# Kernel optimization log

Hardware: AMD Instinct MI355X
Metric: run time of the kernel (lower is better)

The kernel has to match this reference:

```python
import jax, jax.numpy as jnp
import numpy as np

B, T, E, H = 2, 2048, 1024, 16
D = E // H            # head dim = 64
ROT = D // 2          # rotary_dim = 32 (only first half of head dim is rotated)
THETA = 10000.0


def _rope(x):
    # x: (B, H, T, D). Faithful to rotary_embedding_torch.rotate_queries_or_keys
    # with dim=ROT: rotate first ROT features, interleaved-pair style, pass rest.
    t = x.shape[-2]
    inv = 1.0 / (THETA ** (jnp.arange(0, ROT, 2, dtype=jnp.float32) / ROT))   # (ROT//2,)
    freqs = jnp.arange(t, dtype=jnp.float32)[:, None] * inv[None, :]          # (T, ROT//2)
    freqs = jnp.repeat(freqs, 2, axis=-1)                                      # (T, ROT)
    cos, sin = jnp.cos(freqs), jnp.sin(freqs)
    xr, xp = x[..., :ROT], x[..., ROT:]
    p = xr.reshape(*xr.shape[:-1], ROT // 2, 2)
    rot = jnp.stack((-p[..., 1], p[..., 0]), axis=-1).reshape(xr.shape)
    return jnp.concatenate([xr * cos + rot * sin, xp], axis=-1)


def setup_inputs() -> dict:
    key = jax.random.key(0)
    k1, k2, k3 = jax.random.split(key, 3)
    query = jax.random.normal(k1, (B, T, E), dtype=jnp.float32)
    inputs = {
        "query": query,
        "key": query,            # ignored (cross_attention=False)
        "value": query,          # ignored
        "padding_mask": jnp.ones((B, T), dtype=bool),
        "in_proj_weight": jax.random.uniform(k2, (3 * E, E), dtype=jnp.float32),
        "out_proj_weight": jax.random.normal(k3, (E, E), dtype=jnp.float32) * (E ** -0.5),
    }
    return inputs


def reference(query, key, value, padding_mask, in_proj_weight, out_proj_weight):
    # cross_attention=False: key/value are overwritten by query
    key = query
    value = query
    q = query @ in_proj_weight[:E].T
    k = key @ in_proj_weight[E:2 * E].T
    v = value @ in_proj_weight[2 * E:].T
    # NOTE: raw reshape (B,T,E)->(B,H,T,D), exactly as in the torch module
    q = q.reshape(B, H, T, D)
    k = k.reshape(B, H, T, D)
    v = v.reshape(B, H, T, D)
    q = _rope(q)
    k = _rope(k)   # causal self-attention path: rotate keys too
    causal = jnp.tril(jnp.ones((T, T), dtype=bool))                 # (T, T)
    mask = causal[None, None] & padding_mask[:, None, None, :]      # (B,1,T,T) -> broadcast over H
    scores = jnp.einsum("bhqd,bhkd->bhqk", q, k) / jnp.sqrt(jnp.float32(D))
    scores = jnp.where(mask, scores, -jnp.inf)
    attn = jax.nn.softmax(scores, axis=-1)
    x = jnp.einsum("bhqk,bhkd->bhqd", attn, v)
    x = x.reshape(B, T, E)      # raw reshape back, as in torch
    return x @ out_proj_weight.T
```

## Files before the change

### kernel.cpp

```cpp
#include <hip/hip_runtime.h>
#include <stdint.h>

#define T_ 2048
#define E_ 1024

typedef __attribute__((ext_vector_type(8))) __bf16 bf16x8;
typedef __attribute__((ext_vector_type(4))) float f32x4;

__device__ __forceinline__ void gload_lds16(const void* g, void* l) {
  __builtin_amdgcn_global_load_lds(
      (const __attribute__((address_space(1))) unsigned int*)g,
      (__attribute__((address_space(3))) unsigned int*)l, 16, 0, 0);
}

__global__ __launch_bounds__(256) void k_prep(const float4* __restrict__ q,
                                              ushort4* __restrict__ xh,
                                              ushort4* __restrict__ xl,
                                              const float4* __restrict__ win,
                                              ushort4* __restrict__ whh,
                                              ushort4* __restrict__ whl,
                                              const float4* __restrict__ wout,
                                              ushort4* __restrict__ wob,
                                              float2* __restrict__ cs) {
  const int b = blockIdx.x, tid = threadIdx.x;
  if (b < 7168) {
    const float4* src;
    ushort4 *hi, *lo;
    int i;
    if (b < 4096) { src = q; hi = xh; lo = xl; i = b * 256 + tid; }
    else          { src = win; hi = whh; lo = whl; i = (b - 4096) * 256 + tid; }
    float4 x = src[i];
    float xs[4] = {x.x, x.y, x.z, x.w};
    union { __bf16 bb[4]; ushort4 u; } H, L;
#pragma unroll
    for (int jj = 0; jj < 4; ++jj) {
      __bf16 h = (__bf16)xs[jj];
      H.bb[jj] = h;
      L.bb[jj] = (__bf16)(xs[jj] - (float)h);
    }
    hi[i] = H.u;
    lo[i] = L.u;
  } else if (b < 8192) {
    int i = (b - 7168) * 256 + tid;
    float4 x = wout[i];
    float xs[4] = {x.x, x.y, x.z, x.w};
    union { __bf16 bb[4]; ushort4 u; } H;
#pragma unroll
    for (int jj = 0; jj < 4; ++jj) H.bb[jj] = (__bf16)xs[jj];
    wob[i] = H.u;
  } else {
    int i = (b - 8192) * 256 + tid;
    int t = i >> 4, f = i & 15;
    double inv = pow(10000.0, -(double)f / 16.0);
    double ang = (double)t * inv;
    cs[i] = make_float2((float)cos(ang), (float)sin(ang));
  }
}

__global__ __launch_bounds__(256) void k_gemmqk(const __bf16* __restrict__ Ah,
                                                const __bf16* __restrict__ Al,
                                                const __bf16* __restrict__ Bh,
                                                const __bf16* __restrict__ Bl,
                                                int K,
                                                const float2* __restrict__ cs,
                                                __bf16* __restrict__ qhi,
                                                __bf16* __restrict__ qlo,
                                                __bf16* __restrict__ khi,
                                                __bf16* __restrict__ klo) {
  __shared__ __align__(16) __bf16 AsH[128 * 64];
  __shared__ __align__(16) __bf16 BsH[128 * 64];
  __shared__ __align__(16) __bf16 AsL[128 * 64];
  __shared__ __align__(16) __bf16 BsL[128 * 64];
  const int bi = blockIdx.x;
  const int bx = (bi >> 3) & 15;
  const int by = ((bi & 7) << 2) | ((bi >> 7) & 3);
  const int tid = threadIdx.x, lane = tid & 63, w = tid >> 6;
  const int wm = w >> 1, wn = w & 1;
  const int g = lane >> 4, d = lane & 15;
  const int m0 = by * 128, n0 = bx * 128;

  f32x4 acc[4][4];
#pragma unroll
  for (int i = 0; i < 4; ++i)
#pragma unroll
    for (int j = 0; j < 4; ++j) acc[i][j] = (f32x4)(0.0f);

  const int lr8 = lane >> 3;
  const int swz8 = ((lane & 7) ^ lr8) * 8;
  const int rsl = (d & 7);

  for (int k0 = 0; k0 < K; k0 += 64) {
    __syncthreads();
#pragma unroll
    for (int c = 0; c < 4; ++c) {
      const int rr = c * 32 + w * 8 + lr8;
      const int ldo = (c * 32 + w * 8) * 64;
      gload_lds16(Ah + (size_t)(m0 + rr) * K + k0 + swz8, &AsH[ldo]);
      gload_lds16(Al + (size_t)(m0 + rr) * K + k0 + swz8, &AsL[ldo]);
      gload_lds16(Bh + (size_t)(n0 + rr) * K + k0 + swz8, &BsH[ldo]);
      gload_lds16(Bl + (size_t)(n0 + rr) * K + k0 + swz8, &BsL[ldo]);
    }
    __syncthreads();
#pragma unroll
    for (int k2 = 0; k2 < 2; ++k2) {
      const int sl = ((k2 * 4 + g) ^ rsl) * 8;
      bf16x8 bh[4], bl[4];
#pragma unroll
      for (int j = 0; j < 4; ++j) {
        const int r = wn * 64 + j * 16 + d;
        bh[j] = *(const bf16x8*)&BsH[r * 64 + sl];
        bl[j] = *(const bf16x8*)&BsL[r * 64 + sl];
      }
#pragma unroll
      for (int i = 0; i < 4; ++i) {
        const int r = wm * 64 + i * 16 + d;
        const bf16x8 ahf = *(const bf16x8*)&AsH[r * 64 + sl];
        const bf16x8 alf = *(const bf16x8*)&AsL[r * 64 + sl];
#pragma unroll
        for (int j = 0; j < 4; ++j) {
          acc[i][j] = __builtin_amdgcn_mfma_f32_16x16x32_bf16(ahf, bh[j], acc[i][j], 0, 0, 0);
          acc[i][j] = __builtin_amdgcn_mfma_f32_16x16x32_bf16(alf, bh[j], acc[i][j], 0, 0, 0);
          acc[i][j] = __builtin_amdgcn_mfma_f32_16x16x32_bf16(ahf, bl[j], acc[i][j], 0, 0, 0);
        }
      }
    }
  }

#pragma unroll
  for (int i = 0; i < 4; ++i) {
    const int rbase = m0 + wm * 64 + i * 16 + g * 4;
#pragma unroll
    for (int j = 0; j < 4; ++j) {
      const int col = n0 + wn * 64 + j * 16 + d;
#pragma unroll
      for (int r = 0; r < 4; ++r) {
        const float vv = acc[i][j][r];
        const int row = rbase + r;
        const float xp = __shfl_xor(vv, 1);
        const int which = col >> 10;
        const int cl = col & 1023;
        const int d2 = cl & 63;
        const int t2 = (row & 127) * 16 + (cl >> 6);
        float y;
        if (d2 < 32) {
          const float2 cse = cs[t2 * 16 + (d2 >> 1)];
          y = (d2 & 1) ? (vv * cse.x + xp * cse.y) : (vv * cse.x - xp * cse.y);
        } else {
          y = vv;
        }
        if (which == 0) y *= 0.18033688011112042f;
        const __bf16 hi = (__bf16)y;
        const __bf16 lo = (__bf16)(y - (float)hi);
        const size_t off = (size_t)row * 1024 + cl;
        (which ? khi : qhi)[off] = hi;
        (which ? klo : qlo)[off] = lo;
      }
    }
  }
}

template <int EPI>
__global__ __launch_bounds__(256) void k_gemm64(const __bf16* __restrict__ Ah,
                                                const __bf16* __restrict__ Bh,
                                                int N, int K,
                                                __bf16* __restrict__ vt,
                                                float* __restrict__ C32) {
  __shared__ __align__(16) __bf16 As[64 * 64];
  __shared__ __align__(16) __bf16 Bs[128 * 64];
  const int bi = blockIdx.x;
  const int bx = (bi >> 3) & 7;
  const int by = ((bi & 7) << 3) | ((bi >> 6) & 7);
  const int tid = threadIdx.x, lane = tid & 63, w = tid >> 6;
  const int g = lane >> 4, d = lane & 15;
  const int m0 = by * 64, n0 = bx * 128;

  f32x4 acc[4][2];
#pragma unroll
  for (int i = 0; i < 4; ++i)
#pragma unroll
    for (int j = 0; j < 2; ++j) acc[i][j] = (f32x4)(0.0f);

  const int lr8 = lane >> 3;
  const int swz8 = ((lane & 7) ^ lr8) * 8;
  const int rsl = (d & 7);

  for (int k0 = 0; k0 < K; k0 += 64) {
    __syncthreads();
#pragma unroll
    for (int c = 0; c < 2; ++c) {
      const int rr = c * 32 + w * 8 + lr8;
      gload_lds16(Ah + (size_t)(m0 + rr) * K + k0 + swz8, &As[(c * 32 + w * 8) * 64]);
    }
#pragma unroll
    for (int c = 0; c < 4; ++c) {
      const int rr = c * 32 + w * 8 + lr8;
      gload_lds16(Bh + (size_t)(n0 + rr) * K + k0 + swz8, &Bs[(c * 32 + w * 8) * 64]);
    }
    __syncthreads();
#pragma unroll
    for (int k2 = 0; k2 < 2; ++k2) {
      const int sl = ((k2 * 4 + g) ^ rsl) * 8;
      bf16x8 bh[2], ah[4];
#pragma unroll
      for (int j = 0; j < 2; ++j)
        bh[j] = *(const bf16x8*)&Bs[(w * 32 + j * 16 + d) * 64 + sl];
#pragma unroll
      for (int i = 0; i < 4; ++i)
        ah[i] = *(const bf16x8*)&As[(i * 16 + d) * 64 + sl];
#pragma unroll
      for (int i = 0; i < 4; ++i)
#pragma unroll
        for (int j = 0; j < 2; ++j)
          acc[i][j] = __builtin_amdgcn_mfma_f32_16x16x32_bf16(ah[i], bh[j], acc[i][j], 0, 0, 0);
    }
  }

#pragma unroll
  for (int i = 0; i < 4; ++i) {
    const int rbase = m0 + i * 16 + g * 4;
#pragma unroll
    for (int j = 0; j < 2; ++j) {
      const int col = n0 + w * 32 + j * 16 + d;
#pragma unroll
      for (int r = 0; r < 4; ++r) {
        const int row = rbase + r;
        if constexpr (EPI == 1) {
          C32[(size_t)row * N + col] = acc[i][j][r];
        } else {
          const int p = row >> 7;
          const int tp = ((row & 127) << 4) | (col >> 6);
          const int dp = col & 63;
          vt[((size_t)p * 64 + dp) * 2048 + tp] = (__bf16)acc[i][j][r];
        }
      }
    }
  }
}

__global__ __launch_bounds__(512, 4) void k_attn(const __bf16* __restrict__ qhi,
                                                 const __bf16* __restrict__ qlo,
                                                 const __bf16* __restrict__ khi,
                                                 const __bf16* __restrict__ klo,
                                                 const __bf16* __restrict__ v16t,
                                                 __bf16* __restrict__ x16,
                                                 float* __restrict__ po,
                                                 float* __restrict__ pm,
                                                 float* __restrict__ pl_) {
  __shared__ __align__(16) __bf16 KH[2][64 * 64];
  __shared__ __align__(16) __bf16 KL[2][64 * 64];
  __shared__ __align__(16) __bf16 VT[2][64 * 64];
  __shared__ __align__(16) __bf16 PL[8][16 * 72];

  const int bi = blockIdx.x;
  const int b = (bi >> 3) & 15;
  const int panel = (bi & 7) | (((bi >> 7) & 3) << 3);
  const int u0 = 9 * b;
  int qtA = 0;
  while (2 * (qtA + 1) * (qtA + 2) <= u0) ++qtA;
  const int cumA = 2 * qtA * (qtA + 1);
  const int cumB = 2 * (qtA + 1) * (qtA + 2);
  const int jloA = u0 - cumA;
  const bool two = (u0 + 9 > cumB);
  const int jhiA = two ? (cumB - 1 - cumA) : (u0 + 8 - cumA);
  const int jhiB = u0 + 8 - cumB;

  const int tid = threadIdx.x, lane = tid & 63, w = tid >> 6;
  const int g = lane >> 4, d = lane & 15;
  const size_t hb = (size_t)panel * T_ * 64;

  const int kr = tid >> 3, kc = tid & 7;
  const int swz = (kc ^ (kr & 7)) * 8;
  const __bf16* kB = khi + hb;
  const __bf16* lB = klo + hb;
  const __bf16* vB = v16t + (size_t)panel * (64 * T_);

#define STAGE(j, bb)                                                        \
  {                                                                         \
    gload_lds16(kB + (size_t)((j) * 64 + kr) * 64 + swz, &KH[bb][w * 512]); \
    gload_lds16(lB + (size_t)((j) * 64 + kr) * 64 + swz, &KL[bb][w * 512]); \
    gload_lds16(vB + (size_t)kr * T_ + (j) * 64 + swz, &VT[bb][w * 512]);   \
  }

  int cur = 0;
  STAGE(jloA, 0);

  for (int seg = 0; seg < 2; ++seg) {
    if (seg && !two) break;
    const int qt = qtA + seg;
    const int jlo = seg ? 0 : jloA;
    const int jhi = seg ? jhiB : jhiA;
    const int q0 = qt << 8;

    bf16x8 qh[2][2], ql[2][2];
#pragma unroll
    for (int rb = 0; rb < 2; ++rb) {
      const int rbi = w * 2 + rb;
      const size_t qrow = hb + (size_t)(q0 + rbi * 16 + d) * 64;
      qh[rb][0] = *(const bf16x8*)&qhi[qrow + g * 8];
      qh[rb][1] = *(const bf16x8*)&qhi[qrow + 32 + g * 8];
      ql[rb][0] = *(const bf16x8*)&qlo[qrow + g * 8];
      ql[rb][1] = *(const bf16x8*)&qlo[qrow + 32 + g * 8];
    }

    f32x4 o[2][4];
#pragma unroll
    for (int rb = 0; rb < 2; ++rb)
#pragma unroll
      for (int i = 0; i < 4; ++i) o[rb][i] = (f32x4)(0.0f);
    float m_[2] = {-__builtin_inff(), -__builtin_inff()};
    float l_[2] = {0.0f, 0.0f};

    for (int j = jlo; j <= jhi; ++j) {
      __syncthreads();
      if (j < jhi) {
        STAGE(j + 1, cur ^ 1);
      } else if (!seg && two) {
        STAGE(0, cur ^ 1);
      }

#pragma unroll
      for (int rb = 0; rb < 2; ++rb) {
        const int rbi = w * 2 + rb;
        const int qrow0 = q0 + rbi * 16;
        if (j * 64 > qrow0 + 15) continue;

        f32x4 s[4];
        __builtin_amdgcn_s_setprio(1);
#pragma unroll
        for (int f = 0; f < 4; ++f) {
          f32x4 accs = (f32x4)(0.0f);
          const int colr = f * 16 + d;
#pragma unroll
          for (int ds = 0; ds < 2; ++ds) {
            const int slot = ((ds * 4 + g) ^ (colr & 7)) * 8;
            const bf16x8 kf = *(const bf16x8*)&KH[cur][colr * 64 + slot];
            const bf16x8 lf = *(const bf16x8*)&KL[cur][colr * 64 + slot];
            accs = __builtin_amdgcn_mfma_f32_16x16x32_bf16(kf, qh[rb][ds], accs, 0, 0, 0);
            accs = __builtin_amdgcn_mfma_f32_16x16x32_bf16(kf, ql[rb][ds], accs, 0, 0, 0);
            accs = __builtin_amdgcn_mfma_f32_16x16x32_bf16(lf, qh[rb][ds], accs, 0, 0, 0);
          }
          s[f] = accs;
        }
        __builtin_amdgcn_s_setprio(0);

        if (j * 64 + 63 > qrow0) {
          const int qq = qrow0 + d;
#pragma unroll
          for (int f = 0; f < 4; ++f)
#pragma unroll
            for (int r = 0; r < 4; ++r) {
              const int kv = j * 64 + f * 16 + g * 4 + r;
              if (kv > qq) s[f][r] = -30000.0f;
            }
        }

        float pmax = fmaxf(fmaxf(s[0][0], s[0][1]), fmaxf(s[0][2], s[0][3]));
#pragma unroll
        for (int f = 1; f < 4; ++f)
          pmax = fmaxf(pmax, fmaxf(fmaxf(s[f][0], s[f][1]), fmaxf(s[f][2], s[f][3])));
        pmax = fmaxf(pmax, __shfl_xor(pmax, 16));
        pmax = fmaxf(pmax, __shfl_xor(pmax, 32));

        if (!__all(pmax - m_[rb] <= 11.5f)) {
          const float mnew = fmaxf(m_[rb], pmax);
          const float fac = exp2f(m_[rb] - mnew);
          m_[rb] = mnew;
          float facr[4];
#pragma unroll
          for (int r = 0; r < 4; ++r)
            facr[r] = __shfl(fac, (lane & 48) | (g * 4 + r));
#pragma unroll
          for (int ni = 0; ni < 4; ++ni)
#pragma unroll
            for (int r = 0; r < 4; ++r) o[rb][ni][r] *= facr[r];
          l_[rb] *= fac;
        }

        float sum = 0.0f;
#pragma unroll
        for (int f = 0; f < 4; ++f) {
          union { __bf16 bb[4]; ushort4 u4; } pk;
#pragma unroll
          for (int r = 0; r < 4; ++r) {
            const float pv = exp2f(s[f][r] - m_[rb]);
            sum += pv;
            pk.bb[r] = (__bf16)pv;
          }
          *(ushort4*)&PL[w][d * 72 + f * 16 + g * 4] = pk.u4;
        }
        sum += __shfl_xor(sum, 16);
        sum += __shfl_xor(sum, 32);
        l_[rb] += sum;

        __builtin_amdgcn_s_setprio(1);
#pragma unroll
        for (int ks = 0; ks < 2; ++ks) {
          const bf16x8 pa = *(const bf16x8*)&PL[w][d * 72 + ks * 32 + g * 8];
#pragma unroll
          for (int ni = 0; ni < 4; ++ni) {
            const bf16x8 vf =
                *(const bf16x8*)&VT[cur][(ni * 16 + d) * 64 + (((ks * 4 + g) ^ (d & 7)) * 8)];
            o[rb][ni] = __builtin_amdgcn_mfma_f32_16x16x32_bf16(pa, vf, o[rb][ni], 0, 0, 0);
          }
        }
        __builtin_amdgcn_s_setprio(0);
      }
      cur ^= 1;
    }

    if (jlo == 0 && jhi == 4 * qt + 3) {
#pragma unroll
      for (int rb = 0; rb < 2; ++rb) {
        const int rbi = w * 2 + rb;
        float lr[4];
#pragma unroll
        for (int r = 0; r < 4; ++r)
          lr[r] = __shfl(l_[rb], (lane & 48) | (g * 4 + r));
#pragma unroll
        for (int ni = 0; ni < 4; ++ni)
#pragma unroll
          for (int r = 0; r < 4; ++r) {
            const size_t row = hb + (size_t)(q0 + rbi * 16 + g * 4 + r) * 64;
            x16[row + ni * 16 + d] = (__bf16)(o[rb][ni][r] / lr[r]);
          }
      }
    } else {
      const int slot = panel * 23 + b + qt;
#pragma unroll
      for (int rb = 0; rb < 2; ++rb) {
        const int rbi = w * 2 + rb;
#pragma unroll
        for (int ni = 0; ni < 4; ++ni)
#pragma unroll
          for (int r = 0; r < 4; ++r) {
            const int rowin = rbi * 16 + g * 4 + r;
            po[(size_t)slot * 16384 + rowin * 64 + ni * 16 + d] = o[rb][ni][r];
          }
        if (g == 0) {
          pm[slot * 256 + rbi * 16 + d] = m_[rb];
          pl_[slot * 256 + rbi * 16 + d] = l_[rb];
        }
      }
    }
  }
#undef STAGE
}

__global__ __launch_bounds__(256) void k_combine(const float* __restrict__ po,
                                                 const float* __restrict__ pm,
                                                 const float* __restrict__ pl_,
                                                 __bf16* __restrict__ x16) {
  const int p = blockIdx.y;
  const int li = blockIdx.x * 256 + threadIdx.x;
  const int d = li & 63;
  const int t2 = 256 + (li >> 6);
  const int qt = t2 >> 8;
  const int rowin = t2 & 255;
  const int cq = 2 * qt * (qt + 1);
  const int nc = (cq + 4 * qt + 3) / 9 - cq / 9 + 1;
  const int s0 = p * 23 + cq / 9 + qt;
  float M = -__builtin_inff();
  for (int s = 0; s < nc; ++s) M = fmaxf(M, pm[(s0 + s) * 256 + rowin]);
  float L = 0.0f, O = 0.0f;
  for (int s = 0; s < nc; ++s) {
    const float ww = exp2f(pm[(s0 + s) * 256 + rowin] - M);
    L += pl_[(s0 + s) * 256 + rowin] * ww;
    O += po[(size_t)(s0 + s) * 16384 + rowin * 64 + d] * ww;
  }
  x16[((size_t)p * T_ + t2) * 64 + d] = (__bf16)(O / L);
}

extern "C" void kernel_launch(void* const* d_in, const int* in_sizes, int n_in,
                              void* d_out, int out_size, void* d_ws, size_t ws_size,
                              hipStream_t stream) {
  const float* query = (const float*)d_in[0];
  const float* win = (const float*)d_in[4];
  const float* wout = (const float*)d_in[5];
  float* out = (float*)d_out;

  const size_t MB = 1024 * 1024;
  const size_t KB = 1024;
  char* ws = (char*)d_ws;
  __bf16* xh = (__bf16*)(ws);
  __bf16* xl = (__bf16*)(ws + 8 * MB);
  __bf16* v16t = (__bf16*)(ws + 8 * MB);
  __bf16* whh = (__bf16*)(ws + 16 * MB);
  __bf16* whl = (__bf16*)(ws + 22 * MB);
  __bf16* wob = (__bf16*)(ws + 28 * MB);
  float* pm = (float*)(ws + 30 * MB);
  float* pl_ = (float*)(ws + 30 * MB + 768 * KB);
  float2* cs = (float2*)(ws + 31 * MB + 512 * KB);
  float* po = (float*)(ws + 32 * MB);
  __bf16* qhi = (__bf16*)(ws + 78 * MB);
  __bf16* qlo = (__bf16*)(ws + 86 * MB);
  __bf16* khi = (__bf16*)(ws + 94 * MB);
  __bf16* klo = (__bf16*)(ws + 102 * MB);
  __bf16* x16 = (__bf16*)(ws + 78 * MB);

  k_prep<<<8320, 256, 0, stream>>>((const float4*)query, (ushort4*)xh, (ushort4*)xl,
                                   (const float4*)win, (ushort4*)whh, (ushort4*)whl,
                                   (const float4*)wout, (ushort4*)wob, cs);

  k_gemmqk<<<512, 256, 0, stream>>>(xh, xl, whh, whl, 1024, cs, qhi, qlo, khi, klo);

  k_gemm64<2><<<512, 256, 0, stream>>>(xh, whh + (size_t)2048 * 1024, 1024, 1024,
                                       v16t, nullptr);

  k_attn<<<512, 512, 0, stream>>>(qhi, qlo, khi, klo, v16t, x16, po, pm, pl_);

  dim3 gc(448, 32);
  k_combine<<<gc, 256, 0, stream>>>(po, pm, pl_, x16);

  k_gemm64<1><<<512, 256, 0, stream>>>(x16, wob, 1024, 1024, nullptr, out);
}
```

Baseline: 194.3 us.

## Merge QK and V projection GEMMs into one launch, remap combine grid

```diff
diff --git a/kernel.cpp b/kernel.cpp
--- a/kernel.cpp
+++ b/kernel.cpp
@@ -57,114 +57,174 @@
   }
 }
 
-__global__ __launch_bounds__(256) void k_gemmqk(const __bf16* __restrict__ Ah,
-                                                const __bf16* __restrict__ Al,
-                                                const __bf16* __restrict__ Bh,
-                                                const __bf16* __restrict__ Bl,
-                                                int K,
-                                                const float2* __restrict__ cs,
-                                                __bf16* __restrict__ qhi,
-                                                __bf16* __restrict__ qlo,
-                                                __bf16* __restrict__ khi,
-                                                __bf16* __restrict__ klo) {
+__global__ __launch_bounds__(256) void k_proj(const __bf16* __restrict__ xh,
+                                              const __bf16* __restrict__ xl,
+                                              const __bf16* __restrict__ whh,
+                                              const __bf16* __restrict__ whl,
+                                              const float2* __restrict__ cs,
+                                              __bf16* __restrict__ qhi,
+                                              __bf16* __restrict__ qlo,
+                                              __bf16* __restrict__ khi,
+                                              __bf16* __restrict__ klo,
+                                              __bf16* __restrict__ v16t) {
   __shared__ __align__(16) __bf16 AsH[128 * 64];
   __shared__ __align__(16) __bf16 BsH[128 * 64];
   __shared__ __align__(16) __bf16 AsL[128 * 64];
   __shared__ __align__(16) __bf16 BsL[128 * 64];
-  const int bi = blockIdx.x;
-  const int bx = (bi >> 3) & 15;
-  const int by = ((bi & 7) << 2) | ((bi >> 7) & 3);
   const int tid = threadIdx.x, lane = tid & 63, w = tid >> 6;
-  const int wm = w >> 1, wn = w & 1;
   const int g = lane >> 4, d = lane & 15;
-  const int m0 = by * 128, n0 = bx * 128;
-
-  f32x4 acc[4][4];
-#pragma unroll
-  for (int i = 0; i < 4; ++i)
-#pragma unroll
-    for (int j = 0; j < 4; ++j) acc[i][j] = (f32x4)(0.0f);
-
   const int lr8 = lane >> 3;
   const int swz8 = ((lane & 7) ^ lr8) * 8;
-  const int rsl = (d & 7);
-
-  for (int k0 = 0; k0 < K; k0 += 64) {
-    __syncthreads();
-#pragma unroll
-    for (int c = 0; c < 4; ++c) {
-      const int rr = c * 32 + w * 8 + lr8;
-      const int ldo = (c * 32 + w * 8) * 64;
-      gload_lds16(Ah + (size_t)(m0 + rr) * K + k0 + swz8, &AsH[ldo]);
-      gload_lds16(Al + (size_t)(m0 + rr) * K + k0 + swz8, &AsL[ldo]);
-      gload_lds16(Bh + (size_t)(n0 + rr) * K + k0 + swz8, &BsH[ldo]);
-      gload_lds16(Bl + (size_t)(n0 + rr) * K + k0 + swz8, &BsL[ldo]);
-    }
-    __syncthreads();
-#pragma unroll
-    for (int k2 = 0; k2 < 2; ++k2) {
-      const int sl = ((k2 * 4 + g) ^ rsl) * 8;
-      bf16x8 bh[4], bl[4];
+  const int rsl = d & 7;
+  const int K = 1024;
+
+  if (blockIdx.x < 512) {
+    const int bi = blockIdx.x;
+    const int bx = (bi >> 3) & 15;
+    const int by = ((bi & 7) << 2) | ((bi >> 7) & 3);
+    const int wm = w >> 1, wn = w & 1;
+    const int m0 = by * 128, n0 = bx * 128;
+
+    f32x4 acc[4][4];
+#pragma unroll
+    for (int i = 0; i < 4; ++i)
+#pragma unroll
+      for (int j = 0; j < 4; ++j) acc[i][j] = (f32x4)(0.0f);
+
+    for (int k0 = 0; k0 < K; k0 += 64) {
+      __syncthreads();
+#pragma unroll
+      for (int c = 0; c < 4; ++c) {
+        const int rr = c * 32 + w * 8 + lr8;
+        const int ldo = (c * 32 + w * 8) * 64;
+        gload_lds16(xh + (size_t)(m0 + rr) * K + k0 + swz8, &AsH[ldo]);
+        gload_lds16(xl + (size_t)(m0 + rr) * K + k0 + swz8, &AsL[ldo]);
+        gload_lds16(whh + (size_t)(n0 + rr) * K + k0 + swz8, &BsH[ldo]);
+        gload_lds16(whl + (size_t)(n0 + rr) * K + k0 + swz8, &BsL[ldo]);
+      }
+      __syncthreads();
+#pragma unroll
+      for (int k2 = 0; k2 < 2; ++k2) {
+        const int sl = ((k2 * 4 + g) ^ rsl) * 8;
+        bf16x8 bh[4], bl[4];
+#pragma unroll
+        for (int j = 0; j < 4; ++j) {
+          const int r = wn * 64 + j * 16 + d;
+          bh[j] = *(const bf16x8*)&BsH[r * 64 + sl];
+          bl[j] = *(const bf16x8*)&BsL[r * 64 + sl];
+        }
+#pragma unroll
+        for (int i = 0; i < 4; ++i) {
+          const int r = wm * 64 + i * 16 + d;
+          const bf16x8 ahf = *(const bf16x8*)&AsH[r * 64 + sl];
+          const bf16x8 alf = *(const bf16x8*)&AsL[r * 64 + sl];
+#pragma unroll
+          for (int j = 0; j < 4; ++j) {
+            acc[i][j] = __builtin_amdgcn_mfma_f32_16x16x32_bf16(ahf, bh[j], acc[i][j], 0, 0, 0);
+            acc[i][j] = __builtin_amdgcn_mfma_f32_16x16x32_bf16(alf, bh[j], acc[i][j], 0, 0, 0);
+            acc[i][j] = __builtin_amdgcn_mfma_f32_16x16x32_bf16(ahf, bl[j], acc[i][j], 0, 0, 0);
+          }
+        }
+      }
+    }
+
+#pragma unroll
+    for (int i = 0; i < 4; ++i) {
+      const int rbase = m0 + (w >> 1) * 64 + i * 16 + g * 4;
 #pragma unroll
       for (int j = 0; j < 4; ++j) {
-        const int r = wn * 64 + j * 16 + d;
-        bh[j] = *(const bf16x8*)&BsH[r * 64 + sl];
-        bl[j] = *(const bf16x8*)&BsL[r * 64 + sl];
-      }
-#pragma unroll
-      for (int i = 0; i < 4; ++i) {
-        const int r = wm * 64 + i * 16 + d;
-        const bf16x8 ahf = *(const bf16x8*)&AsH[r * 64 + sl];
-        const bf16x8 alf = *(const bf16x8*)&AsL[r * 64 + sl];
-#pragma unroll
-        for (int j = 0; j < 4; ++j) {
-          acc[i][j] = __builtin_amdgcn_mfma_f32_16x16x32_bf16(ahf, bh[j], acc[i][j], 0, 0, 0);
-          acc[i][j] = __builtin_amdgcn_mfma_f32_16x16x32_bf16(alf, bh[j], acc[i][j], 0, 0, 0);
-          acc[i][j] = __builtin_amdgcn_mfma_f32_16x16x32_bf16(ahf, bl[j], acc[i][j], 0, 0, 0);
-        }
-      }
-    }
-  }
-
-#pragma unroll
-  for (int i = 0; i < 4; ++i) {
-    const int rbase = m0 + wm * 64 + i * 16 + g * 4;
-#pragma unroll
-    for (int j = 0; j < 4; ++j) {
-      const int col = n0 + wn * 64 + j * 16 + d;
-#pragma unroll
-      for (int r = 0; r < 4; ++r) {
-        const float vv = acc[i][j][r];
-        const int row = rbase + r;
-        const float xp = __shfl_xor(vv, 1);
-        const int which = col >> 10;
-        const int cl = col & 1023;
-        const int d2 = cl & 63;
-        const int t2 = (row & 127) * 16 + (cl >> 6);
-        float y;
-        if (d2 < 32) {
-          const float2 cse = cs[t2 * 16 + (d2 >> 1)];
-          y = (d2 & 1) ? (vv * cse.x + xp * cse.y) : (vv * cse.x - xp * cse.y);
-        } else {
-          y = vv;
-        }
-        if (which == 0) y *= 0.18033688011112042f;
-        const __bf16 hi = (__bf16)y;
-        const __bf16 lo = (__bf16)(y - (float)hi);
-        const size_t off = (size_t)row * 1024 + cl;
-        (which ? khi : qhi)[off] = hi;
-        (which ? klo : qlo)[off] = lo;
-      }
-    }
-  }
-}
-
-template <int EPI>
-__global__ __launch_bounds__(256) void k_gemm64(const __bf16* __restrict__ Ah,
-                                                const __bf16* __restrict__ Bh,
-                                                int N, int K,
-                                                __bf16* __restrict__ vt,
-                                                float* __restrict__ C32) {
+        const int col = n0 + (w & 1) * 64 + j * 16 + d;
+#pragma unroll
+        for (int r = 0; r < 4; ++r) {
+          const float vv = acc[i][j][r];
+          const int row = rbase + r;
+          const float xp = __shfl_xor(vv, 1);
+          const int which = col >> 10;
+          const int cl = col & 1023;
+          const int d2 = cl & 63;
+          const int t2 = (row & 127) * 16 + (cl >> 6);
+          float y;
+          if (d2 < 32) {
+            const float2 cse = cs[t2 * 16 + (d2 >> 1)];
+            y = (d2 & 1) ? (vv * cse.x + xp * cse.y) : (vv * cse.x - xp * cse.y);
+          } else {
+            y = vv;
+          }
+          if (which == 0) y *= 0.18033688011112042f;
+          const __bf16 hi = (__bf16)y;
+          const __bf16 lo = (__bf16)(y - (float)hi);
+          const size_t off = (size_t)row * 1024 + cl;
+          (which ? khi : qhi)[off] = hi;
+          (which ? klo : qlo)[off] = lo;
+        }
+      }
+    }
+  } else {
+    const int bi = blockIdx.x - 512;
+    const int bx = (bi >> 3) & 7;
+    const int by = ((bi & 7) << 3) | ((bi >> 6) & 7);
+    const int m0 = by * 64, n0 = bx * 128;
+    const __bf16* Bv = whh + (size_t)2048 * 1024;
+
+    f32x4 acc[4][2];
+#pragma unroll
+    for (int i = 0; i < 4; ++i)
+#pragma unroll
+      for (int j = 0; j < 2; ++j) acc[i][j] = (f32x4)(0.0f);
+
+    for (int k0 = 0; k0 < K; k0 += 64) {
+      __syncthreads();
+#pragma unroll
+      for (int c = 0; c < 2; ++c) {
+        const int rr = c * 32 + w * 8 + lr8;
+        gload_lds16(xh + (size_t)(m0 + rr) * K + k0 + swz8, &AsH[(c * 32 + w * 8) * 64]);
+      }
+#pragma unroll
+      for (int c = 0; c < 4; ++c) {
+        const int rr = c * 32 + w * 8 + lr8;
+        gload_lds16(Bv + (size_t)(n0 + rr) * K + k0 + swz8, &BsH[(c * 32 + w * 8) * 64]);
+      }
+      __syncthreads();
+#pragma unroll
+      for (int k2 = 0; k2 < 2; ++k2) {
+        const int sl = ((k2 * 4 + g) ^ rsl) * 8;
+        bf16x8 bh[2], ah[4];
+#pragma unroll
+        for (int j = 0; j < 2; ++j)
+          bh[j] = *(const bf16x8*)&BsH[(w * 32 + j * 16 + d) * 64 + sl];
+#pragma unroll
+        for (int i = 0; i < 4; ++i)
+          ah[i] = *(const bf16x8*)&AsH[(i * 16 + d) * 64 + sl];
+#pragma unroll
+        for (int i = 0; i < 4; ++i)
+#pragma unroll
+          for (int j = 0; j < 2; ++j)
+            acc[i][j] = __builtin_amdgcn_mfma_f32_16x16x32_bf16(ah[i], bh[j], acc[i][j], 0, 0, 0);
+      }
+    }
+
+#pragma unroll
+    for (int i = 0; i < 4; ++i) {
+      const int rbase = m0 + i * 16 + g * 4;
+#pragma unroll
+      for (int j = 0; j < 2; ++j) {
+        const int col = n0 + w * 32 + j * 16 + d;
+#pragma unroll
+        for (int r = 0; r < 4; ++r) {
+          const int row = rbase + r;
+          const int p = row >> 7;
+          const int tp = ((row & 127) << 4) | (col >> 6);
+          const int dp = col & 63;
+          v16t[((size_t)p * 64 + dp) * 2048 + tp] = (__bf16)acc[i][j][r];
+        }
+      }
+    }
+  }
+}
+
+__global__ __launch_bounds__(256) void k_gemmout(const __bf16* __restrict__ Ah,
+                                                 const __bf16* __restrict__ Bh,
+                                                 float* __restrict__ C32) {
   __shared__ __align__(16) __bf16 As[64 * 64];
   __shared__ __align__(16) __bf16 Bs[128 * 64];
   const int bi = blockIdx.x;
@@ -173,6 +233,7 @@
   const int tid = threadIdx.x, lane = tid & 63, w = tid >> 6;
   const int g = lane >> 4, d = lane & 15;
   const int m0 = by * 64, n0 = bx * 128;
+  const int K = 1024, N = 1024;
 
   f32x4 acc[4][2];
 #pragma unroll
@@ -182,7 +243,7 @@
 
   const int lr8 = lane >> 3;
   const int swz8 = ((lane & 7) ^ lr8) * 8;
-  const int rsl = (d & 7);
+  const int rsl = d & 7;
 
   for (int k0 = 0; k0 < K; k0 += 64) {
     __syncthreads();
@@ -222,17 +283,8 @@
     for (int j = 0; j < 2; ++j) {
       const int col = n0 + w * 32 + j * 16 + d;
 #pragma unroll
-      for (int r = 0; r < 4; ++r) {
-        const int row = rbase + r;
-        if constexpr (EPI == 1) {
-          C32[(size_t)row * N + col] = acc[i][j][r];
-        } else {
-          const int p = row >> 7;
-          const int tp = ((row & 127) << 4) | (col >> 6);
-          const int dp = col & 63;
-          vt[((size_t)p * 64 + dp) * 2048 + tp] = (__bf16)acc[i][j][r];
-        }
-      }
+      for (int r = 0; r < 4; ++r)
+        C32[(size_t)(rbase + r) * N + col] = acc[i][j][r];
     }
   }
 }
@@ -450,8 +502,9 @@
                                                  const float* __restrict__ pm,
                                                  const float* __restrict__ pl_,
                                                  __bf16* __restrict__ x16) {
-  const int p = blockIdx.y;
-  const int li = blockIdx.x * 256 + threadIdx.x;
+  const int bi = blockIdx.x;
+  const int p = (bi & 7) | ((bi / 3584) << 3);
+  const int li = ((bi >> 3) % 448) * 256 + threadIdx.x;
   const int d = li & 63;
   const int t2 = 256 + (li >> 6);
   const int qt = t2 >> 8;
@@ -483,33 +536,29 @@
   char* ws = (char*)d_ws;
   __bf16* xh = (__bf16*)(ws);
   __bf16* xl = (__bf16*)(ws + 8 * MB);
-  __bf16* v16t = (__bf16*)(ws + 8 * MB);
   __bf16* whh = (__bf16*)(ws + 16 * MB);
   __bf16* whl = (__bf16*)(ws + 22 * MB);
-  __bf16* wob = (__bf16*)(ws + 28 * MB);
-  float* pm = (float*)(ws + 30 * MB);
-  float* pl_ = (float*)(ws + 30 * MB + 768 * KB);
-  float2* cs = (float2*)(ws + 31 * MB + 512 * KB);
-  float* po = (float*)(ws + 32 * MB);
-  __bf16* qhi = (__bf16*)(ws + 78 * MB);
-  __bf16* qlo = (__bf16*)(ws + 86 * MB);
-  __bf16* khi = (__bf16*)(ws + 94 * MB);
-  __bf16* klo = (__bf16*)(ws + 102 * MB);
-  __bf16* x16 = (__bf16*)(ws + 78 * MB);
+  float* po = (float*)(ws);
+  __bf16* v16t = (__bf16*)(ws + 46 * MB);
+  __bf16* qhi = (__bf16*)(ws + 54 * MB);
+  __bf16* qlo = (__bf16*)(ws + 62 * MB);
+  __bf16* khi = (__bf16*)(ws + 70 * MB);
+  __bf16* klo = (__bf16*)(ws + 78 * MB);
+  __bf16* wob = (__bf16*)(ws + 86 * MB);
+  float* pm = (float*)(ws + 88 * MB);
+  float* pl_ = (float*)(ws + 88 * MB + 768 * KB);
+  float2* cs = (float2*)(ws + 89 * MB + 512 * KB);
+  __bf16* x16 = (__bf16*)(ws + 54 * MB);
 
   k_prep<<<8320, 256, 0, stream>>>((const float4*)query, (ushort4*)xh, (ushort4*)xl,
                                    (const float4*)win, (ushort4*)whh, (ushort4*)whl,
                                    (const float4*)wout, (ushort4*)wob, cs);
 
-  k_gemmqk<<<512, 256, 0, stream>>>(xh, xl, whh, whl, 1024, cs, qhi, qlo, khi, klo);
-
-  k_gemm64<2><<<512, 256, 0, stream>>>(xh, whh + (size_t)2048 * 1024, 1024, 1024,
-                                       v16t, nullptr);
+  k_proj<<<1024, 256, 0, stream>>>(xh, xl, whh, whl, cs, qhi, qlo, khi, klo, v16t);
 
   k_attn<<<512, 512, 0, stream>>>(qhi, qlo, khi, klo, v16t, x16, po, pm, pl_);
 
-  dim3 gc(448, 32);
-  k_combine<<<gc, 256, 0, stream>>>(po, pm, pl_, x16);
-
-  k_gemm64<1><<<512, 256, 0, stream>>>(x16, wob, 1024, 1024, nullptr, out);
-}
+  k_combine<<<14336, 256, 0, stream>>>(po, pm, pl_, x16);
+
+  k_gemmout<<<512, 256, 0, stream>>>(x16, wob, out);
+}
```

After: 186.7 us. -3.9%, faster.
